# Performance work log

Measured on AMD Instinct MI355X. Metric: run time of the kernel, lower is better.

## Reference

```python
import jax, jax.numpy as jnp
import numpy as np

VOCAB = 50257
D_EMBED = 512
RES = 2048
D_SPARSE = 32            # avg nnz per row -> density gamma = D_SPARSE / RES
R_OUT = 512
B, T = 8, 256
SIGMA_IN = 1.0
RHO = 0.99


def _sparse_dense(key, shape, density, scale):
    """Dense matrix emulating torch sparse_coo with given density (mask*randn*scale)."""
    k1, k2 = jax.random.split(key)
    vals = jax.random.normal(k1, shape, dtype=jnp.float32) * scale
    mask = jax.random.uniform(k2, shape) < density
    return jnp.where(mask, vals, 0.0)


def setup_inputs() -> dict:
    key = jax.random.key(0)
    ks = jax.random.split(key, 9)
    gamma = D_SPARSE / RES
    x = jax.random.randint(ks[0], (B, T), 0, VOCAB)
    tok_emb = jax.random.normal(ks[1], (VOCAB, D_EMBED), dtype=jnp.float32) * 0.02
    # W_in: [d_embed, reservoir], sparse density gamma, scale sigma_in (stored transposed in torch)
    W_in = _sparse_dense(ks[2], (D_EMBED, RES), gamma, SIGMA_IN)
    # W_rec: sparse gaussian scaled so spectral radius ~ RHO (radius of sparse gaussian ~ sqrt(N*gamma))
    W_rec = _sparse_dense(ks[3], (RES, RES), gamma, 1.0) * (RHO / np.sqrt(RES * gamma))
    a = jax.random.uniform(ks[4], (RES,), dtype=jnp.float32)  # leak rates in [alpha_min, alpha_max]
    Wb = jax.random.normal(ks[5], (R_OUT, RES), dtype=jnp.float32) / np.sqrt(RES)
    Wa = jax.random.normal(ks[6], (VOCAB, R_OUT), dtype=jnp.float32) / np.sqrt(R_OUT)
    bias = jnp.zeros((VOCAB,), dtype=jnp.float32)
    h0 = jnp.zeros((RES,), dtype=jnp.float32)
    return dict(x=x, tok_emb=tok_emb, W_in=W_in, W_rec=W_rec, a=a,
                Wb=Wb, Wa=Wa, bias=bias, h0=h0)


def reference(x, tok_emb, W_in, W_rec, a, Wb, Wa, bias, h0):
    # embedding + input projection hoisted out of the time loop (no state dependency)
    emb = tok_emb[x]                                    # [B,T,D_EMBED]
    emb_proj = jnp.einsum('btd,dr->btr', emb, W_in)     # [B,T,RES]
    h_init = jnp.broadcast_to(h0, (x.shape[0], h0.shape[0]))  # [B,RES]

    def step(h, ep_t):
        rec = h @ W_rec.T                               # sparse mm(W_rec, h^T)^T
        pre = jnp.clip(ep_t + rec, -10.0, 10.0)
        h_new = (1.0 - a) * h + a * jnp.tanh(pre)
        return h_new, h_new

    _, hs = jax.lax.scan(step, h_init, jnp.swapaxes(emb_proj, 0, 1))  # [T,B,RES]
    hs = jnp.swapaxes(hs, 0, 1)                         # [B,T,RES]
    # readout A(drop(B(h))); dropout is identity in eval
    proj = jnp.einsum('btr,pr->btp', hs, Wb)            # [B,T,R_OUT]
    logits = jnp.einsum('btp,vp->btv', proj, Wa) + bias  # [B,T,VOCAB]
    return logits
```

## Files before the change

### kernel.cpp

```cpp
#include <hip/hip_runtime.h>
#include <hip/hip_bf16.h>
#include <stdint.h>

#define VOCAB 50257
#define VPAD  50304
#define DEMB  512
#define RES   2048
#define ROUT  512
#define BB    8
#define TT    256
#define BT    2048
#define SLOTS 80
#define RBLK  32
#define UPB   64

typedef _Float16 half8 __attribute__((ext_vector_type(8)));
typedef float f32x4 __attribute__((ext_vector_type(4)));

__device__ __forceinline__ void g2lds16(const _Float16* g, _Float16* l) {
  __builtin_amdgcn_global_load_lds((const __attribute__((address_space(1))) void*)g,
                                   (__attribute__((address_space(3))) void*)l,
                                   16, 0, 0);
}

__global__ __launch_bounds__(256)
void prep_k(const int* __restrict__ x, const float* __restrict__ temb,
            const float* __restrict__ Win, const float* __restrict__ Wb,
            const float* __restrict__ Wa, const float* __restrict__ h0,
            _Float16* __restrict__ Aemb, _Float16* __restrict__ Wt,
            _Float16* __restrict__ Wb16, _Float16* __restrict__ Wa16,
            _Float16* __restrict__ hbuf) {
  const int gt = blockIdx.x * 256 + threadIdx.x;
  const int gs = gridDim.x * 256;
  for (int i = gt; i < BT * DEMB; i += gs) {
    int bt = i >> 9, d = i & 511;
    Aemb[i] = (_Float16)temb[(size_t)x[bt] * DEMB + d];
  }
  for (int i = gt; i < RES * DEMB; i += gs) {
    int rr = i >> 9, d = i & 511;
    Wt[i] = (_Float16)Win[(size_t)d * RES + rr];
  }
  for (int i = gt; i < ROUT * RES; i += gs) Wb16[i] = (_Float16)Wb[i];
  for (int i = gt; i < VPAD * ROUT; i += gs)
    Wa16[i] = (i < VOCAB * ROUT) ? (_Float16)Wa[i] : (_Float16)0.f;
  for (int i = gt; i < RES * BB; i += gs) hbuf[i] = (_Float16)h0[i >> 3];
}

__global__ __launch_bounds__(256)
void build_ell_k(const float* __restrict__ Wrec, float* __restrict__ evals,
                 unsigned short* __restrict__ ecols, int* __restrict__ ecnt) {
  __shared__ int base;
  const int r = blockIdx.x;
  if (threadIdx.x == 0) base = 0;
  __syncthreads();
  const float* row = Wrec + (size_t)r * RES;
  const int lane = threadIdx.x & 63;
  for (int j0 = 0; j0 < RES; j0 += 256) {
    int j = j0 + threadIdx.x;
    float v = row[j];
    bool nz = (v != 0.f);
    unsigned long long mask = __ballot(nz);
    int pre = __popcll(mask & ((1ull << lane) - 1ull));
    int tot = __popcll(mask);
    int wb = 0;
    if (lane == 0 && tot) wb = atomicAdd(&base, tot);
    wb = __shfl(wb, 0);
    if (nz) {
      int slot = wb + pre;
      if (slot < SLOTS) {
        evals[(size_t)r * SLOTS + slot] = v;
        ecols[(size_t)r * SLOTS + slot] = (unsigned short)j;
      }
    }
  }
  __syncthreads();
  if (threadIdx.x == 0) ecnt[r] = (base <= SLOTS) ? base : SLOTS;
}

__global__ __launch_bounds__(256)
void recurrence_k(const float* __restrict__ ep, const float* __restrict__ evals,
                  const unsigned short* __restrict__ ecols, const int* __restrict__ ecnt,
                  const float* __restrict__ a, const float* __restrict__ h0,
                  _Float16* __restrict__ hbuf, _Float16* __restrict__ hs,
                  int* __restrict__ scnt) {
  __shared__ __align__(16) _Float16 hcur[RES * BB];
  __shared__ float vals[UPB * (SLOTS + 1)];
  __shared__ unsigned short cols[UPB * (SLOTS + 1)];
  __shared__ float hown[UPB][BB];
  __shared__ float aa[UPB];
  __shared__ int cnts[UPB];

  const int tid = threadIdx.x;
  const int u0 = blockIdx.x * UPB;
  const int ul = tid >> 2;
  const int g  = tid & 3;

  for (int i = tid; i < UPB * SLOTS; i += 256) {
    int u = i / SLOTS, s = i - u * SLOTS;
    vals[u * (SLOTS + 1) + s] = evals[(size_t)(u0 + u) * SLOTS + s];
    cols[u * (SLOTS + 1) + s] = ecols[(size_t)(u0 + u) * SLOTS + s];
  }
  if (tid < UPB) { aa[tid] = a[u0 + tid]; cnts[tid] = ecnt[u0 + tid]; }
  for (int i = tid; i < UPB * BB; i += 256) hown[i >> 3][i & 7] = h0[u0 + (i >> 3)];
  __syncthreads();

  for (int t = 0; t < TT; ++t) {
    if (t > 0) {
      if (tid == 0) {
        while (__hip_atomic_load(&scnt[t], __ATOMIC_RELAXED, __HIP_MEMORY_SCOPE_AGENT) < RBLK)
          __builtin_amdgcn_s_sleep(4);
        __threadfence();
      }
      __syncthreads();
    }
    {
      const _Float16* src = hbuf + (size_t)(t & 1) * (RES * BB);
      #pragma unroll
      for (int r = 0; r < 8; ++r)
        g2lds16(src + (r * 256 + tid) * 8, hcur + (r * 256 + (tid & ~63)) * 8);
    }
    __syncthreads();

    float acc[BB];
    #pragma unroll
    for (int b = 0; b < BB; ++b) acc[b] = 0.f;
    const int ns = cnts[ul];
    for (int s = g; s < ns; s += 4) {
      float wv = vals[ul * (SLOTS + 1) + s];
      int c = cols[ul * (SLOTS + 1) + s];
      half8 hv = *(const half8*)(hcur + c * BB);
      #pragma unroll
      for (int b = 0; b < BB; ++b) acc[b] += wv * (float)hv[b];
    }
    #pragma unroll
    for (int b = 0; b < BB; ++b) {
      acc[b] += __shfl_xor(acc[b], 1);
      acc[b] += __shfl_xor(acc[b], 2);
    }
    _Float16* dst = hbuf + (size_t)((t + 1) & 1) * (RES * BB);
    #pragma unroll
    for (int q = 0; q < 2; ++q) {
      int b = 2 * g + q;
      float epv = ep[((size_t)b * TT + t) * RES + u0 + ul];
      float pre = epv + acc[b];
      pre = fminf(10.f, fmaxf(-10.f, pre));
      float al = aa[ul];
      float hn = (1.f - al) * hown[ul][b] + al * tanhf(pre);
      hown[ul][b] = hn;
      _Float16 h16 = (_Float16)hn;
      dst[(size_t)(u0 + ul) * BB + b] = h16;
      hs[((size_t)b * TT + t) * RES + u0 + ul] = h16;
    }
    __syncthreads();
    if (tid == 0) {
      __threadfence();
      __hip_atomic_fetch_add(&scnt[t + 1], 1, __ATOMIC_RELAXED, __HIP_MEMORY_SCOPE_AGENT);
    }
  }
}

template <int MODE>
__global__ __launch_bounds__(256)
void gemm_bt(const _Float16* __restrict__ A, const _Float16* __restrict__ B,
             float* __restrict__ Cf, _Float16* __restrict__ Ch,
             const float* __restrict__ bias, int Nld, int Ncheck, int K) {
  __shared__ __align__(16) _Float16 sA[128 * 64];
  __shared__ __align__(16) _Float16 sB[128 * 64];
  const int tid = threadIdx.x;
  const int m0 = blockIdx.x * 128, n0 = blockIdx.y * 128;
  const int lane = tid & 63, w = tid >> 6;
  const int wm = (w & 1) << 6, wn = (w >> 1) << 6;
  const int lrow = lane & 15, quad = lane >> 4;

  f32x4 acc[4][4];
  #pragma unroll
  for (int i = 0; i < 4; ++i)
    #pragma unroll
    for (int j = 0; j < 4; ++j) acc[i][j] = (f32x4){0.f, 0.f, 0.f, 0.f};

  const _Float16* Ab = A + (size_t)m0 * K;
  const _Float16* Bb = B + (size_t)n0 * K;
  const int kt_n = K >> 6;
  for (int kt = 0; kt < kt_n; ++kt) {
    const int k0 = kt << 6;
    #pragma unroll
    for (int r = 0; r < 4; ++r) {
      int s = (r << 8) + tid;
      int row = s >> 3;
      int k8 = (s & 7) ^ (row & 7);
      g2lds16(Ab + (size_t)row * K + k0 + (k8 << 3), sA + ((s & ~63) << 3));
      g2lds16(Bb + (size_t)row * K + k0 + (k8 << 3), sB + ((s & ~63) << 3));
    }
    __syncthreads();
    #pragma unroll
    for (int kk = 0; kk < 2; ++kk) {
      half8 af[4], bf[4];
      #pragma unroll
      for (int i = 0; i < 4; ++i) {
        int ra = wm + (i << 4) + lrow;
        af[i] = *(const half8*)(sA + (((ra << 3) + (((kk << 2) + quad) ^ (ra & 7))) << 3));
        int rb = wn + (i << 4) + lrow;
        bf[i] = *(const half8*)(sB + (((rb << 3) + (((kk << 2) + quad) ^ (rb & 7))) << 3));
      }
      #pragma unroll
      for (int i = 0; i < 4; ++i)
        #pragma unroll
        for (int j = 0; j < 4; ++j)
          acc[i][j] = __builtin_amdgcn_mfma_f32_16x16x32_f16(af[i], bf[j], acc[i][j], 0, 0, 0);
    }
    __syncthreads();
  }
  #pragma unroll
  for (int i = 0; i < 4; ++i) {
    const int row = m0 + wm + (i << 4) + (quad << 2);
    #pragma unroll
    for (int j = 0; j < 4; ++j) {
      const int col = n0 + wn + (j << 4) + lrow;
      f32x4 v = acc[i][j];
      if (MODE == 1) {
        if (col < Ncheck) {
          const float bv = bias[col];
          #pragma unroll
          for (int r2 = 0; r2 < 4; ++r2)
            Cf[(size_t)(row + r2) * Nld + col] = v[r2] + bv;
        }
      } else if (MODE == 0) {
        #pragma unroll
        for (int r2 = 0; r2 < 4; ++r2) Cf[(size_t)(row + r2) * Nld + col] = v[r2];
      } else {
        #pragma unroll
        for (int r2 = 0; r2 < 4; ++r2) Ch[(size_t)(row + r2) * Nld + col] = (_Float16)v[r2];
      }
    }
  }
}

extern "C" void kernel_launch(void* const* d_in, const int* in_sizes, int n_in,
                              void* d_out, int out_size, void* d_ws, size_t ws_size,
                              hipStream_t stream) {
  const int*   x    = (const int*)d_in[0];
  const float* temb = (const float*)d_in[1];
  const float* Win  = (const float*)d_in[2];
  const float* Wrec = (const float*)d_in[3];
  const float* a    = (const float*)d_in[4];
  const float* Wb   = (const float*)d_in[5];
  const float* Wa   = (const float*)d_in[6];
  const float* bias = (const float*)d_in[7];
  const float* h0   = (const float*)d_in[8];
  float* out = (float*)d_out;
  (void)in_sizes; (void)n_in; (void)out_size; (void)ws_size;

  char* p = (char*)d_ws;
  auto take = [&](size_t bytes) -> char* {
    char* r = p;
    p += (bytes + 255) & ~(size_t)255;
    return r;
  };
  _Float16* Aemb = (_Float16*)take((size_t)BT * DEMB * 2);
  _Float16* Wt   = (_Float16*)take((size_t)RES * DEMB * 2);
  _Float16* Wb16 = (_Float16*)take((size_t)ROUT * RES * 2);
  _Float16* Wa16 = (_Float16*)take((size_t)VPAD * ROUT * 2);
  _Float16* proj = (_Float16*)take((size_t)BT * ROUT * 2);
  float*    ep   = (float*)   take((size_t)BT * RES * 4);
  _Float16* hs   = (_Float16*)take((size_t)BT * RES * 2);
  _Float16* hbuf = (_Float16*)take((size_t)2 * RES * BB * 2);
  float*    evals= (float*)   take((size_t)RES * SLOTS * 4);
  unsigned short* ecols = (unsigned short*)take((size_t)RES * SLOTS * 2);
  int*      ecnt = (int*)take((size_t)RES * 4);
  int*      scnt = (int*)take((size_t)(TT + 1) * 4);

  hipMemsetAsync(scnt, 0, (TT + 1) * sizeof(int), stream);
  prep_k<<<dim3(2048), 256, 0, stream>>>(x, temb, Win, Wb, Wa, h0, Aemb, Wt, Wb16, Wa16, hbuf);
  build_ell_k<<<dim3(RES), 256, 0, stream>>>(Wrec, evals, ecols, ecnt);
  gemm_bt<0><<<dim3(16, 16), 256, 0, stream>>>(Aemb, Wt, ep, nullptr, nullptr, RES, RES, DEMB);
  recurrence_k<<<dim3(RBLK), 256, 0, stream>>>(ep, evals, ecols, ecnt, a, h0, hbuf, hs, scnt);
  gemm_bt<2><<<dim3(16, 4), 256, 0, stream>>>(hs, Wb16, nullptr, proj, nullptr, ROUT, ROUT, RES);
  gemm_bt<1><<<dim3(16, 393), 256, 0, stream>>>(proj, Wa16, out, nullptr, bias, VOCAB, VOCAB, ROUT);
}
```

Baseline: 2.177 ms.

## Run recurrence one block per batch with register-resident sparse chunks

Replaces the multi-block recurrence, which synchronised 32 blocks through global atomics at every timestep, with one 512-thread block per batch element that keeps the full state in LDS. A new chunkify kernel splits each sparse row into 16-nonzero chunks with packed byte offsets, and each thread holds up to eight chunks' weights and columns in registers. Partial row sums are combined with LDS float atomics. This removes the inter-block spin barrier at every timestep, but uses only 8 blocks, carries heavy register pressure and atomic contention, and swaps tanhf for an exp-based approximation.

New measurement: 4.460 ms. +104.9%, slower.

```diff
diff --git a/kernel.cpp b/kernel.cpp
--- a/kernel.cpp
+++ b/kernel.cpp
@@ -11,10 +11,11 @@
 #define TT    256
 #define BT    2048
 #define SLOTS 80
-#define RBLK  32
-#define UPB   64
+#define NCAP  8192
+#define NREG  8
 
 typedef _Float16 half8 __attribute__((ext_vector_type(8)));
+typedef _Float16 h4v   __attribute__((ext_vector_type(4)));
 typedef float f32x4 __attribute__((ext_vector_type(4)));
 
 __device__ __forceinline__ void g2lds16(const _Float16* g, _Float16* l) {
@@ -26,10 +27,9 @@
 __global__ __launch_bounds__(256)
 void prep_k(const int* __restrict__ x, const float* __restrict__ temb,
             const float* __restrict__ Win, const float* __restrict__ Wb,
-            const float* __restrict__ Wa, const float* __restrict__ h0,
+            const float* __restrict__ Wa,
             _Float16* __restrict__ Aemb, _Float16* __restrict__ Wt,
-            _Float16* __restrict__ Wb16, _Float16* __restrict__ Wa16,
-            _Float16* __restrict__ hbuf) {
+            _Float16* __restrict__ Wb16, _Float16* __restrict__ Wa16) {
   const int gt = blockIdx.x * 256 + threadIdx.x;
   const int gs = gridDim.x * 256;
   for (int i = gt; i < BT * DEMB; i += gs) {
@@ -43,7 +43,6 @@
   for (int i = gt; i < ROUT * RES; i += gs) Wb16[i] = (_Float16)Wb[i];
   for (int i = gt; i < VPAD * ROUT; i += gs)
     Wa16[i] = (i < VOCAB * ROUT) ? (_Float16)Wa[i] : (_Float16)0.f;
-  for (int i = gt; i < RES * BB; i += gs) hbuf[i] = (_Float16)h0[i >> 3];
 }
 
 __global__ __launch_bounds__(256)
@@ -78,84 +77,135 @@
 }
 
 __global__ __launch_bounds__(256)
-void recurrence_k(const float* __restrict__ ep, const float* __restrict__ evals,
-                  const unsigned short* __restrict__ ecols, const int* __restrict__ ecnt,
-                  const float* __restrict__ a, const float* __restrict__ h0,
-                  _Float16* __restrict__ hbuf, _Float16* __restrict__ hs,
-                  int* __restrict__ scnt) {
-  __shared__ __align__(16) _Float16 hcur[RES * BB];
-  __shared__ float vals[UPB * (SLOTS + 1)];
-  __shared__ unsigned short cols[UPB * (SLOTS + 1)];
-  __shared__ float hown[UPB][BB];
-  __shared__ float aa[UPB];
-  __shared__ int cnts[UPB];
-
+void chunkify_k(const float* __restrict__ evals, const unsigned short* __restrict__ ecols,
+                const int* __restrict__ ecnt, float* __restrict__ ckval,
+                unsigned int* __restrict__ ckcolp, unsigned short* __restrict__ ckrow,
+                int* __restrict__ ncnt) {
+  const int r = blockIdx.x * 256 + threadIdx.x;
+  if (r >= RES) return;
+  const int cnt = ecnt[r];
+  const int nc = (cnt + 15) >> 4;
+  if (nc == 0) return;
+  const int base = atomicAdd(ncnt, nc);
+  for (int c = 0; c < nc; ++c) {
+    const int cc = base + c;
+    if (cc >= NCAP) break;
+    ckrow[cc] = (unsigned short)(r * 4);
+    unsigned int lo = 0;
+    for (int j = 0; j < 16; ++j) {
+      const int idx = c * 16 + j;
+      float v = 0.f; unsigned int c2 = 0;
+      if (idx < cnt) {
+        v  = evals[(size_t)r * SLOTS + idx];
+        c2 = (unsigned int)ecols[(size_t)r * SLOTS + idx] * 2u;
+      }
+      ckval[(size_t)j * NCAP + cc] = v;
+      if ((j & 1) == 0) lo = c2;
+      else ckcolp[(size_t)(j >> 1) * NCAP + cc] = lo | (c2 << 16);
+    }
+  }
+}
+
+__global__ __launch_bounds__(512, 2)
+void rec2_k(const float* __restrict__ ep, const float* __restrict__ ckval,
+            const unsigned int* __restrict__ ckcolp, const unsigned short* __restrict__ ckrow,
+            const int* __restrict__ ncnt, const float* __restrict__ a,
+            const float* __restrict__ h0, _Float16* __restrict__ hs) {
+  __shared__ __align__(16) _Float16 h16[RES];
+  __shared__ __align__(16) float rowbuf[RES];
   const int tid = threadIdx.x;
-  const int u0 = blockIdx.x * UPB;
-  const int ul = tid >> 2;
-  const int g  = tid & 3;
-
-  for (int i = tid; i < UPB * SLOTS; i += 256) {
-    int u = i / SLOTS, s = i - u * SLOTS;
-    vals[u * (SLOTS + 1) + s] = evals[(size_t)(u0 + u) * SLOTS + s];
-    cols[u * (SLOTS + 1) + s] = ecols[(size_t)(u0 + u) * SLOTS + s];
-  }
-  if (tid < UPB) { aa[tid] = a[u0 + tid]; cnts[tid] = ecnt[u0 + tid]; }
-  for (int i = tid; i < UPB * BB; i += 256) hown[i >> 3][i & 7] = h0[u0 + (i >> 3)];
+  const int bb  = blockIdx.x;
+  const int NC  = *ncnt;
+
+  float        wv[NREG * 16];
+  unsigned int wc[NREG * 8];
+  int          rowoff[NREG];
+  #pragma unroll
+  for (int s = 0; s < NREG; ++s) {
+    const int c = s * 512 + tid;
+    const bool ok = (c < NC);
+    rowoff[s] = ok ? (int)ckrow[c] : 0;
+    #pragma unroll
+    for (int j = 0; j < 16; ++j)
+      wv[s * 16 + j] = ok ? ckval[(size_t)j * NCAP + c] : 0.f;
+    #pragma unroll
+    for (int p = 0; p < 8; ++p)
+      wc[s * 8 + p] = ok ? ckcolp[(size_t)p * NCAP + c] : 0u;
+  }
+
+  const int u0 = tid * 4;
+  float hown[4], au[4];
+  {
+    const f32x4 hv = *(const f32x4*)(h0 + u0);
+    const f32x4 av = *(const f32x4*)(a + u0);
+    h4v hi;
+    #pragma unroll
+    for (int q = 0; q < 4; ++q) { hown[q] = hv[q]; au[q] = av[q]; hi[q] = (_Float16)hv[q]; }
+    *(h4v*)(h16 + u0) = hi;
+    *(f32x4*)(rowbuf + u0) = (f32x4){0.f, 0.f, 0.f, 0.f};
+  }
   __syncthreads();
 
+  const float*    epp = ep + (size_t)bb * TT * RES + u0;
+  _Float16*       hsp = hs + (size_t)bb * TT * RES + u0;
+
   for (int t = 0; t < TT; ++t) {
-    if (t > 0) {
-      if (tid == 0) {
-        while (__hip_atomic_load(&scnt[t], __ATOMIC_RELAXED, __HIP_MEMORY_SCOPE_AGENT) < RBLK)
-          __builtin_amdgcn_s_sleep(4);
-        __threadfence();
-      }
-      __syncthreads();
-    }
-    {
-      const _Float16* src = hbuf + (size_t)(t & 1) * (RES * BB);
+    const f32x4 epv = *(const f32x4*)epp;
+
+    #pragma unroll
+    for (int s = 0; s < NREG; ++s) {
+      float a0 = 0.f, a1 = 0.f, a2 = 0.f, a3 = 0.f;
       #pragma unroll
-      for (int r = 0; r < 8; ++r)
-        g2lds16(src + (r * 256 + tid) * 8, hcur + (r * 256 + (tid & ~63)) * 8);
+      for (int p = 0; p < 8; ++p) {
+        const unsigned int w = wc[s * 8 + p];
+        const _Float16 hA = *(const _Float16*)((const char*)h16 + (w & 0xffffu));
+        const _Float16 hB = *(const _Float16*)((const char*)h16 + (w >> 16));
+        if ((p & 1) == 0) {
+          a0 = fmaf(wv[s * 16 + 2 * p],     (float)hA, a0);
+          a1 = fmaf(wv[s * 16 + 2 * p + 1], (float)hB, a1);
+        } else {
+          a2 = fmaf(wv[s * 16 + 2 * p],     (float)hA, a2);
+          a3 = fmaf(wv[s * 16 + 2 * p + 1], (float)hB, a3);
+        }
+      }
+      const float fs = (a0 + a1) + (a2 + a3);
+      if (fs != 0.f) atomicAdd((float*)((char*)rowbuf + rowoff[s]), fs);
+    }
+    for (int c = NREG * 512 + tid; c < NC; c += 512) {
+      const int ro = (int)ckrow[c];
+      float b0 = 0.f, b1 = 0.f;
+      #pragma unroll
+      for (int p = 0; p < 8; ++p) {
+        const unsigned int w = ckcolp[(size_t)p * NCAP + c];
+        const float v0 = ckval[(size_t)(2 * p) * NCAP + c];
+        const float v1 = ckval[(size_t)(2 * p + 1) * NCAP + c];
+        const _Float16 hA = *(const _Float16*)((const char*)h16 + (w & 0xffffu));
+        const _Float16 hB = *(const _Float16*)((const char*)h16 + (w >> 16));
+        b0 = fmaf(v0, (float)hA, b0);
+        b1 = fmaf(v1, (float)hB, b1);
+      }
+      const float fs = b0 + b1;
+      if (fs != 0.f) atomicAdd((float*)((char*)rowbuf + ro), fs);
     }
     __syncthreads();
 
-    float acc[BB];
-    #pragma unroll
-    for (int b = 0; b < BB; ++b) acc[b] = 0.f;
-    const int ns = cnts[ul];
-    for (int s = g; s < ns; s += 4) {
-      float wv = vals[ul * (SLOTS + 1) + s];
-      int c = cols[ul * (SLOTS + 1) + s];
-      half8 hv = *(const half8*)(hcur + c * BB);
-      #pragma unroll
-      for (int b = 0; b < BB; ++b) acc[b] += wv * (float)hv[b];
-    }
-    #pragma unroll
-    for (int b = 0; b < BB; ++b) {
-      acc[b] += __shfl_xor(acc[b], 1);
-      acc[b] += __shfl_xor(acc[b], 2);
-    }
-    _Float16* dst = hbuf + (size_t)((t + 1) & 1) * (RES * BB);
-    #pragma unroll
-    for (int q = 0; q < 2; ++q) {
-      int b = 2 * g + q;
-      float epv = ep[((size_t)b * TT + t) * RES + u0 + ul];
-      float pre = epv + acc[b];
+    const f32x4 rs = *(f32x4*)(rowbuf + u0);
+    *(f32x4*)(rowbuf + u0) = (f32x4){0.f, 0.f, 0.f, 0.f};
+    h4v ho;
+    #pragma unroll
+    for (int q = 0; q < 4; ++q) {
+      float pre = epv[q] + rs[q];
       pre = fminf(10.f, fmaxf(-10.f, pre));
-      float al = aa[ul];
-      float hn = (1.f - al) * hown[ul][b] + al * tanhf(pre);
-      hown[ul][b] = hn;
-      _Float16 h16 = (_Float16)hn;
-      dst[(size_t)(u0 + ul) * BB + b] = h16;
-      hs[((size_t)b * TT + t) * RES + u0 + ul] = h16;
-    }
+      const float z  = __expf(2.f * pre);
+      const float th = __fdividef(z - 1.f, z + 1.f);
+      const float hn = fmaf(au[q], th - hown[q], hown[q]);
+      hown[q] = hn;
+      ho[q] = (_Float16)hn;
+    }
+    *(h4v*)(h16 + u0) = ho;
+    *(h4v*)hsp = ho;
     __syncthreads();
-    if (tid == 0) {
-      __threadfence();
-      __hip_atomic_fetch_add(&scnt[t + 1], 1, __ATOMIC_RELAXED, __HIP_MEMORY_SCOPE_AGENT);
-    }
+    epp += RES; hsp += RES;
   }
 }
 
@@ -263,17 +313,20 @@
   _Float16* proj = (_Float16*)take((size_t)BT * ROUT * 2);
   float*    ep   = (float*)   take((size_t)BT * RES * 4);
   _Float16* hs   = (_Float16*)take((size_t)BT * RES * 2);
-  _Float16* hbuf = (_Float16*)take((size_t)2 * RES * BB * 2);
   float*    evals= (float*)   take((size_t)RES * SLOTS * 4);
   unsigned short* ecols = (unsigned short*)take((size_t)RES * SLOTS * 2);
   int*      ecnt = (int*)take((size_t)RES * 4);
-  int*      scnt = (int*)take((size_t)(TT + 1) * 4);
-
-  hipMemsetAsync(scnt, 0, (TT + 1) * sizeof(int), stream);
-  prep_k<<<dim3(2048), 256, 0, stream>>>(x, temb, Win, Wb, Wa, h0, Aemb, Wt, Wb16, Wa16, hbuf);
+  int*      ncnt = (int*)take(256);
+  float*    ckval = (float*)take((size_t)16 * NCAP * 4);
+  unsigned int* ckcolp = (unsigned int*)take((size_t)8 * NCAP * 4);
+  unsigned short* ckrow = (unsigned short*)take((size_t)NCAP * 2);
+
+  hipMemsetAsync(ncnt, 0, sizeof(int), stream);
+  prep_k<<<dim3(2048), 256, 0, stream>>>(x, temb, Win, Wb, Wa, Aemb, Wt, Wb16, Wa16);
   build_ell_k<<<dim3(RES), 256, 0, stream>>>(Wrec, evals, ecols, ecnt);
+  chunkify_k<<<dim3(RES / 256), 256, 0, stream>>>(evals, ecols, ecnt, ckval, ckcolp, ckrow, ncnt);
   gemm_bt<0><<<dim3(16, 16), 256, 0, stream>>>(Aemb, Wt, ep, nullptr, nullptr, RES, RES, DEMB);
-  recurrence_k<<<dim3(RBLK), 256, 0, stream>>>(ep, evals, ecols, ecnt, a, h0, hbuf, hs, scnt);
+  rec2_k<<<dim3(BB), 512, 0, stream>>>(ep, ckval, ckcolp, ckrow, ncnt, a, h0, hs);
   gemm_bt<2><<<dim3(16, 4), 256, 0, stream>>>(hs, Wb16, nullptr, proj, nullptr, ROUT, ROUT, RES);
   gemm_bt<1><<<dim3(16, 393), 256, 0, stream>>>(proj, Wa16, out, nullptr, bias, VOCAB, VOCAB, ROUT);
 }
```
